# Kernel optimization log

Measured on AMD Instinct MI355X. Metric: run time of the kernel, lower is better.

Reference implementation:

```python
import jax, jax.numpy as jnp
import numpy as np

B, T, HE, L, HD = 512, 512, 512, 64, 512

def setup_inputs() -> dict:
    key = jax.random.key(0)
    ks = jax.random.split(key, 16)
    def w(k, shape):
        return jax.random.normal(k, shape, dtype=jnp.float32) * 0.05
    z32 = lambda n: jnp.zeros((n,), jnp.float32)
    return {
        "input_tensor": jax.random.normal(ks[0], (B, T, 1), dtype=jnp.float32),
        # encoder LSTMCell (keras gate order i, f, g, o)
        "enc_W": w(ks[1], (1, 4 * HE)),
        "enc_U": w(ks[2], (HE, 4 * HE)),
        "enc_b": z32(4 * HE),
        # encoder mu / std heads
        "emu_W": w(ks[3], (HE, L)), "emu_b": z32(L),
        "estd_W": w(ks[4], (HE, L)), "estd_b": z32(L),
        # decoder first-state dense (tanh)
        "dfs_W": w(ks[5], (L, HD)), "dfs_b": z32(HD),
        # decoder LSTMCell
        "dec_W": w(ks[6], (L, 4 * HD)),
        "dec_U": w(ks[7], (HD, 4 * HD)),
        "dec_b": z32(4 * HD),
        # decoder mu / std heads (Dense(1))
        "dmu_W": w(ks[8], (HD, 1)), "dmu_b": z32(1),
        "dstd_W": w(ks[9], (HD, 1)), "dstd_b": z32(1),
    }

def _lstm_update(gates, c):
    i, f, g, o = jnp.split(gates, 4, axis=-1)
    c_new = jax.nn.sigmoid(f) * c + jax.nn.sigmoid(i) * jnp.tanh(g)
    h_new = jax.nn.sigmoid(o) * jnp.tanh(c_new)
    return h_new, c_new

def reference(input_tensor, enc_W, enc_U, enc_b, emu_W, emu_b, estd_W, estd_b,
              dfs_W, dfs_b, dec_W, dec_U, dec_b, dmu_W, dmu_b, dstd_W, dstd_b):
    x = input_tensor
    Bn, Tn = x.shape[0], x.shape[1]
    He = enc_U.shape[0]

    # ---- encoder: LSTM over time, keep final h ----
    def enc_step(carry, xt):
        h, c = carry
        gates = xt @ enc_W + h @ enc_U + enc_b
        return _lstm_update(gates, c), None
    h0 = jnp.zeros((Bn, He), x.dtype)
    (hT, _), _ = jax.lax.scan(enc_step, (h0, h0), jnp.swapaxes(x, 0, 1))

    mu_enc = hT @ emu_W + emu_b                       # [B, L]
    sigma_enc = jax.nn.softplus(hT @ estd_W + estd_b)  # [B, L]
    z = mu_enc  # call() uses reparam=False -> latent returns mu

    # ---- decoder: LSTM fed constant z each step ----
    hd = jnp.tanh(z @ dfs_W + dfs_b)                  # [B, HD]
    cd = jnp.zeros_like(hd)
    zin = z @ dec_W + dec_b                           # input projection constant over t
    def dec_step(carry, _):
        h, c = carry
        h_new, c_new = _lstm_update(zin + h @ dec_U, c)
        mu = h_new @ dmu_W + dmu_b                    # [B, 1]
        sg = h_new @ dstd_W + dstd_b
        return (h_new, c_new), (mu, sg)
    _, (mus, sgs) = jax.lax.scan(dec_step, (hd, cd), None, length=Tn)

    mu_dec = jnp.swapaxes(mus, 0, 1)                  # [B, T, 1]
    sigma_dec = jax.nn.softplus(jnp.swapaxes(sgs, 0, 1))
    return (mu_dec, sigma_dec, mu_enc, sigma_enc)
```

## Files before the change

kernel.cpp:

```cpp
#include <hip/hip_runtime.h>


#define B_   512
#define T_   512
#define H_   512
#define NGR  32
#define WPG  8
#define RPG  16
#define UPW  64

typedef _Float16 f16;
typedef _Float16 f16x8 __attribute__((ext_vector_type(8)));
typedef _Float16 f16x4 __attribute__((ext_vector_type(4)));
typedef float f32x16 __attribute__((ext_vector_type(16)));
typedef unsigned long long u64;

#define OFF_SG_DEC 262144
#define OFF_MU_ENC 524288
#define OFF_SG_ENC 557056

__device__ __forceinline__ float sigm_(float x) { return 1.f / (1.f + __expf(-x)); }
__device__ __forceinline__ float tanh_(float x) {
  float t = fabsf(x);
  float e = __expf(2.f * t);
  float r = 1.f - 2.f / (e + 1.f);
  return x < 0.f ? -r : r;
}
__device__ __forceinline__ float softplus_(float x) {
  return fmaxf(x, 0.f) + log1pf(__expf(-fabsf(x)));
}

__global__ void pack_U(const float* __restrict__ U, f16* __restrict__ Upk) {
  const int e = blockIdx.x * 256 + threadIdx.x;
  const int j = e & 7, lane = (e >> 3) & 63, ks = (e >> 9) & 31;
  const int w = (e >> 14) & 7, wg = (e >> 17) & 7;
  const int ccol = lane & 31, khalf = lane >> 5;
  const int uu = ccol >> 2, gate = ccol & 3;
  const int k = ks * 16 + khalf * 8 + j;
  const int gcol = gate * 512 + wg * UPW + w * 8 + uu;
  Upk[e] = (f16)U[k * 2048 + gcol];
}

template <int IS_DEC>
__global__ void __launch_bounds__(512, 1)
lstm_rec(const f16* __restrict__ Upk,
         const float* __restrict__ xin,
         const float* __restrict__ wa,
         const float* __restrict__ wb,
         f16* __restrict__ hbuf,
         float* __restrict__ accmu,
         float* __restrict__ accsg,
         int* __restrict__ flags) {
  const int bid = blockIdx.x;
  const int wg = (bid >> 3) & 7;
  const int g = (bid & 7) * 4 + (bid >> 6);
  const int tid = threadIdx.x;
  const int wave = tid >> 6, lane = tid & 63;
  const int R0 = g * RPG;
  const int U0 = wg * UPW;

  const int ccol = lane & 31, khalf = lane >> 5;
  f16x8 Breg[32];
#pragma unroll
  for (int ks = 0; ks < 32; ++ks) {
    const f16* p = Upk + (((wg * 8 + wave) * 32 + ks) << 9) + lane * 8;
    asm volatile("global_load_dwordx4 %0, %1, off\n\ts_waitcnt vmcnt(0)"
                 : "=v"(Breg[ks]) : "v"(p));
  }

  const int row = tid >> 4;
  const int q = (tid & 15) * 4;
  float addv[16], xw[16], dmur[4], dstdr[4];
  if (tid < 256) {
#pragma unroll
    for (int m = 0; m < 4; ++m) {
#pragma unroll
      for (int gt = 0; gt < 4; ++gt) {
        const int col = gt * 512 + U0 + q + m;
        if (IS_DEC) {
          addv[m * 4 + gt] = xin[(R0 + row) * 2048 + col];
          xw[m * 4 + gt] = 0.f;
        } else {
          addv[m * 4 + gt] = wb[col];
          xw[m * 4 + gt] = wa[col];
        }
      }
      if (IS_DEC) {
        dmur[m] = wa[U0 + q + m];
        dstdr[m] = wb[U0 + q + m];
      } else {
        dmur[m] = 0.f;
        dstdr[m] = 0.f;
      }
    }
  }

  float cst[4] = {0.f, 0.f, 0.f, 0.f};

  __shared__ __align__(16) f16 hstage[RPG * 536];
  __shared__ float gatesLds[RPG * 260];
  __shared__ float xl[RPG * 516];

  if (!IS_DEC) {
#pragma unroll
    for (int i = 0; i < 16; ++i) {
      const int idx = tid + i * 512;
      const int r = idx >> 9, c2 = idx & 511;
      xl[r * 516 + c2] = xin[(R0 + r) * T_ + c2];
    }
    __syncthreads();
  }

  const int hrow = lane & 15;
  int* const myflag = &flags[(g * WPG + wg) * 32];
  int* const grpflags = &flags[(g * WPG) * 32];

  for (int t = 0; t < T_; ++t) {
    if (t) {
      for (;;) {
        int fv = t;
        if (lane < WPG)
          fv = __hip_atomic_load(&grpflags[lane * 32], __ATOMIC_RELAXED,
                                 __HIP_MEMORY_SCOPE_AGENT);
        if (__all(fv >= t)) break;
        asm volatile("s_sleep 1");
      }
    }

    const u64* hsrc64 = (const u64*)(hbuf + (t & 1) * (B_ * H_) + R0 * H_);
#pragma unroll
    for (int i = 0; i < 4; ++i) {
      const int w = tid + i * 512;
      const int r = w >> 7, c8 = w & 127;
      u64 v = __hip_atomic_load(hsrc64 + w, __ATOMIC_RELAXED,
                                __HIP_MEMORY_SCOPE_AGENT);
      *(u64*)&hstage[r * 536 + c8 * 4] = v;
    }
    __syncthreads();

    f32x16 acc;
#pragma unroll
    for (int j = 0; j < 16; ++j) acc[j] = 0.f;
#pragma unroll
    for (int ks = 0; ks < 32; ++ks) {
      f16x8 a = *(const f16x8*)&hstage[hrow * 536 + ks * 16 + khalf * 8];
      acc = __builtin_amdgcn_mfma_f32_32x32x16_f16(a, Breg[ks], acc, 0, 0, 0);
    }
#pragma unroll
    for (int r = 0; r < 8; ++r) {
      const int orow = (r & 3) + 8 * (r >> 2) + 4 * khalf;
      gatesLds[orow * 260 + wave * 32 + ccol] = acc[r];
    }
    __syncthreads();

    float hn[4];
    if (tid < 256) {
      float xv = 0.f;
      if (!IS_DEC) xv = xl[row * 516 + t];
#pragma unroll
      for (int m = 0; m < 4; ++m) {
        float ga[4];
#pragma unroll
        for (int gt = 0; gt < 4; ++gt) {
          float v = gatesLds[row * 260 + (q + m) * 4 + gt] + addv[m * 4 + gt];
          if (!IS_DEC) v += xv * xw[m * 4 + gt];
          ga[gt] = v;
        }
        const float iv = sigm_(ga[0]);
        const float fv = sigm_(ga[1]);
        const float gv = tanh_(ga[2]);
        const float ov = sigm_(ga[3]);
        const float cn = fv * cst[m] + iv * gv;
        cst[m] = cn;
        hn[m] = ov * tanh_(cn);
      }
      union { f16x4 h4; u64 u; } cv;
#pragma unroll
      for (int m = 0; m < 4; ++m) cv.h4[m] = (f16)hn[m];
      f16* hdst = hbuf + ((t + 1) & 1) * (B_ * H_) + (R0 + row) * H_ + U0 + q;
      __hip_atomic_store((u64*)hdst, cv.u, __ATOMIC_RELAXED,
                         __HIP_MEMORY_SCOPE_AGENT);
    }

    asm volatile("s_waitcnt vmcnt(0)" ::: "memory");
    __syncthreads();
    if (t + 1 < T_ && tid == 0)
      __hip_atomic_store(myflag, t + 1, __ATOMIC_RELAXED,
                         __HIP_MEMORY_SCOPE_AGENT);

    if (IS_DEC && tid < 256) {
      float pmu = 0.f, psg = 0.f;
#pragma unroll
      for (int m = 0; m < 4; ++m) {
        pmu += (float)((f16)hn[m]) * dmur[m];
        psg += (float)((f16)hn[m]) * dstdr[m];
      }
#pragma unroll
      for (int o = 1; o < 16; o <<= 1) {
        pmu += __shfl_xor(pmu, o);
        psg += __shfl_xor(psg, o);
      }
      if ((tid & 15) == 0) {
        unsafeAtomicAdd(&accmu[(R0 + row) * T_ + t], pmu);
        unsafeAtomicAdd(&accsg[(R0 + row) * T_ + t], psg);
      }
    }
  }
}

__global__ void enc_heads(const f16* __restrict__ h0, const float* __restrict__ emuW,
                          const float* __restrict__ emub, const float* __restrict__ estdW,
                          const float* __restrict__ estdb, float* __restrict__ out,
                          float* __restrict__ z) {
  const int b = blockIdx.x, tid = threadIdx.x;
  __shared__ float hrow[512];
  for (int k = tid; k < 512; k += 128)
    hrow[k] = (float)h0[b * H_ + k];
  __syncthreads();
  const int head = tid >> 6, l = tid & 63;
  const float* W = head ? estdW : emuW;
  float a = 0.f;
#pragma unroll 8
  for (int k = 0; k < 512; ++k) a += hrow[k] * W[k * 64 + l];
  if (head == 0) {
    const float v = a + emub[l];
    out[OFF_MU_ENC + b * 64 + l] = v;
    z[b * 64 + l] = v;
  } else {
    out[OFF_SG_ENC + b * 64 + l] = softplus_(a + estdb[l]);
  }
}

__global__ void dec_prep(const float* __restrict__ z, const float* __restrict__ dfsW,
                         const float* __restrict__ dfsb, const float* __restrict__ decW,
                         const float* __restrict__ decb, f16* __restrict__ hbuf,
                         float* __restrict__ zin) {
  const int b = blockIdx.x, tid = threadIdx.x;
  __shared__ float zl[64];
  if (tid < 64) zl[tid] = z[b * 64 + tid];
  __syncthreads();
  for (int c = tid; c < 512; c += 256) {
    float a = dfsb[c];
#pragma unroll
    for (int l = 0; l < 64; ++l) a += zl[l] * dfsW[l * 512 + c];
    hbuf[b * H_ + c] = (f16)tanh_(a);
  }
  for (int c = tid; c < 2048; c += 256) {
    float a = decb[c];
#pragma unroll
    for (int l = 0; l < 64; ++l) a += zl[l] * decW[l * 2048 + c];
    zin[b * 2048 + c] = a;
  }
}

__global__ void finalize_k(const float* __restrict__ accmu, const float* __restrict__ accsg,
                           const float* __restrict__ dmub, const float* __restrict__ dstdb,
                           float* __restrict__ out) {
  const int i = blockIdx.x * 256 + threadIdx.x;
  out[i] = accmu[i] + dmub[0];
  out[OFF_SG_DEC + i] = softplus_(accsg[i] + dstdb[0]);
}

extern "C" void kernel_launch(void* const* d_in, const int* in_sizes, int n_in,
                              void* d_out, int out_size, void* d_ws, size_t ws_size,
                              hipStream_t stream) {
  (void)in_sizes; (void)n_in; (void)out_size; (void)ws_size;
  const float* x     = (const float*)d_in[0];
  const float* encW  = (const float*)d_in[1];
  const float* encU  = (const float*)d_in[2];
  const float* encb  = (const float*)d_in[3];
  const float* emuW  = (const float*)d_in[4];
  const float* emub  = (const float*)d_in[5];
  const float* estdW = (const float*)d_in[6];
  const float* estdb = (const float*)d_in[7];
  const float* dfsW  = (const float*)d_in[8];
  const float* dfsb  = (const float*)d_in[9];
  const float* decW  = (const float*)d_in[10];
  const float* decU  = (const float*)d_in[11];
  const float* decb  = (const float*)d_in[12];
  const float* dmuW  = (const float*)d_in[13];
  const float* dmub  = (const float*)d_in[14];
  const float* dstdW = (const float*)d_in[15];
  const float* dstdb = (const float*)d_in[16];

  char* ws = (char*)d_ws;
  f16* hbuf    = (f16*)(ws + 0);
  float* accmu = (float*)(ws + (1u << 20));
  float* accsg = (float*)(ws + (2u << 20));
  int* flags   = (int*)(ws + (3u << 20));
  f16* UpkE    = (f16*)(ws + (3u << 20) + 65536);
  float* zin   = (float*)(ws + (3u << 20) + 65536);
  f16* UpkD    = (f16*)(ws + (7u << 20) + 65536);
  float* z     = (float*)(ws + (9u << 20) + 65536);
  float* out   = (float*)d_out;

  hipMemsetAsync(d_ws, 0, (3u << 20) + 65536, stream);

  hipLaunchKernelGGL(pack_U, dim3(4096), dim3(256), 0, stream, encU, UpkE);
  hipLaunchKernelGGL(pack_U, dim3(4096), dim3(256), 0, stream, decU, UpkD);

  hipLaunchKernelGGL((lstm_rec<0>), dim3(256), dim3(512), 0, stream,
                     UpkE, x, encW, encb, hbuf, (float*)nullptr, (float*)nullptr,
                     flags);
  hipLaunchKernelGGL(enc_heads, dim3(512), dim3(128), 0, stream,
                     hbuf, emuW, emub, estdW, estdb, out, z);
  hipLaunchKernelGGL(dec_prep, dim3(512), dim3(256), 0, stream,
                     z, dfsW, dfsb, decW, decb, hbuf, zin);
  hipLaunchKernelGGL((lstm_rec<1>), dim3(256), dim3(512), 0, stream,
                     UpkD, zin, dmuW, dstdW, hbuf, accmu, accsg, flags + 8192);
  hipLaunchKernelGGL(finalize_k, dim3(1024), dim3(256), 0, stream,
                     accmu, accsg, dmub, dstdb, out);
}
```

Before: 4.403 ms.

## Interleave two row groups per block to overlap flag waits with MFMA work

Each workgroup now handles two independent 16-row batch groups (A and B) and alternates between them. While one group's MFMA and gate math run, the block waits for and prefetches the other group's hidden state, which hides the cross-block flag spin and global h loads behind compute. The grid is halved from 256 to 128 blocks, so fewer CUs are used and each block does twice the serial work per timestep. Latency hiding could be outweighed by the longer per-step critical path.

```diff
diff --git a/kernel.cpp b/kernel.cpp
--- a/kernel.cpp
+++ b/kernel.cpp
@@ -4,7 +4,6 @@
 #define B_   512
 #define T_   512
 #define H_   512
-#define NGR  32
 #define WPG  8
 #define RPG  16
 #define UPW  64
@@ -53,24 +52,24 @@
          int* __restrict__ flags) {
   const int bid = blockIdx.x;
   const int wg = (bid >> 3) & 7;
-  const int g = (bid & 7) * 4 + (bid >> 6);
+  const int p = (bid & 7) * 2 + (bid >> 6);
+  const int RA = p * 16, RB = (p + 16) * 16;
   const int tid = threadIdx.x;
   const int wave = tid >> 6, lane = tid & 63;
-  const int R0 = g * RPG;
   const int U0 = wg * UPW;
 
   const int ccol = lane & 31, khalf = lane >> 5;
   f16x8 Breg[32];
 #pragma unroll
   for (int ks = 0; ks < 32; ++ks) {
-    const f16* p = Upk + (((wg * 8 + wave) * 32 + ks) << 9) + lane * 8;
+    const f16* ptr = Upk + (((wg * 8 + wave) * 32 + ks) << 9) + lane * 8;
     asm volatile("global_load_dwordx4 %0, %1, off\n\ts_waitcnt vmcnt(0)"
-                 : "=v"(Breg[ks]) : "v"(p));
+                 : "=v"(Breg[ks]) : "v"(ptr));
   }
 
   const int row = tid >> 4;
   const int q = (tid & 15) * 4;
-  float addv[16], xw[16], dmur[4], dstdr[4];
+  float addA[16], addB[16], xw[16], dmur[4], dstdr[4];
   if (tid < 256) {
 #pragma unroll
     for (int m = 0; m < 4; ++m) {
@@ -78,10 +77,12 @@
       for (int gt = 0; gt < 4; ++gt) {
         const int col = gt * 512 + U0 + q + m;
         if (IS_DEC) {
-          addv[m * 4 + gt] = xin[(R0 + row) * 2048 + col];
+          addA[m * 4 + gt] = xin[(RA + row) * 2048 + col];
+          addB[m * 4 + gt] = xin[(RB + row) * 2048 + col];
           xw[m * 4 + gt] = 0.f;
         } else {
-          addv[m * 4 + gt] = wb[col];
+          addA[m * 4 + gt] = wb[col];
+          addB[m * 4 + gt] = wb[col];
           xw[m * 4 + gt] = wa[col];
         }
       }
@@ -89,63 +90,81 @@
         dmur[m] = wa[U0 + q + m];
         dstdr[m] = wb[U0 + q + m];
       } else {
-        dmur[m] = 0.f;
-        dstdr[m] = 0.f;
-      }
-    }
-  }
-
-  float cst[4] = {0.f, 0.f, 0.f, 0.f};
-
-  __shared__ __align__(16) f16 hstage[RPG * 536];
+        dmur[m] = 0.f; dstdr[m] = 0.f;
+      }
+    }
+  }
+
+  float cstA[4] = {0.f, 0.f, 0.f, 0.f};
+  float cstB[4] = {0.f, 0.f, 0.f, 0.f};
+
+  __shared__ __align__(16) f16 bufA[RPG * 536];
+  __shared__ __align__(16) f16 bufB[RPG * 536];
   __shared__ float gatesLds[RPG * 260];
-  __shared__ float xl[RPG * 516];
+  __shared__ float xl[IS_DEC ? 4 : 32 * 516];
 
   if (!IS_DEC) {
 #pragma unroll
-    for (int i = 0; i < 16; ++i) {
+    for (int i = 0; i < 32; ++i) {
       const int idx = tid + i * 512;
       const int r = idx >> 9, c2 = idx & 511;
-      xl[r * 516 + c2] = xin[(R0 + r) * T_ + c2];
-    }
-    __syncthreads();
-  }
-
+      const int grow = (r < 16) ? (RA + r) : (RB + r - 16);
+      xl[r * 516 + c2] = xin[grow * T_ + c2];
+    }
+  }
+
+  int srow[4], scol[4], wof[4];
+#pragma unroll
+  for (int i = 0; i < 4; ++i) {
+    const int w = tid + i * 512;
+    srow[i] = w >> 7; scol[i] = w & 127;
+    wof[i] = w;
+  }
+  const u64* hb64 = (const u64*)hbuf;
+  const int baseA = RA * 128, baseB = RB * 128;
   const int hrow = lane & 15;
-  int* const myflag = &flags[(g * WPG + wg) * 32];
-  int* const grpflags = &flags[(g * WPG) * 32];
+
+  int* const flagA = &flags[(p * WPG + wg) * 32];
+  int* const flagB = &flags[((p + 16) * WPG + wg) * 32];
+  const int* const gfA = &flags[(p * WPG) * 32];
+  const int* const gfB = &flags[((p + 16) * WPG) * 32];
+
+#pragma unroll
+  for (int i = 0; i < 4; ++i) {
+    u64 v = __hip_atomic_load(hb64 + baseA + wof[i], __ATOMIC_RELAXED,
+                              __HIP_MEMORY_SCOPE_AGENT);
+    *(u64*)&bufA[srow[i] * 536 + scol[i] * 4] = v;
+  }
+  __syncthreads();
 
   for (int t = 0; t < T_; ++t) {
+    const int b0 = (t & 1) ? 65536 : 0;
+    const int b1 = (t & 1) ? 0 : 65536;
+    const int last = (t + 1 == T_);
+
+    f32x16 acc;
+#pragma unroll
+    for (int jj = 0; jj < 16; ++jj) acc[jj] = 0.f;
+#pragma unroll
+    for (int ks = 0; ks < 32; ++ks) {
+      f16x8 a = *(const f16x8*)&bufA[hrow * 536 + ks * 16 + khalf * 8];
+      acc = __builtin_amdgcn_mfma_f32_32x32x16_f16(a, Breg[ks], acc, 0, 0, 0);
+    }
     if (t) {
       for (;;) {
         int fv = t;
         if (lane < WPG)
-          fv = __hip_atomic_load(&grpflags[lane * 32], __ATOMIC_RELAXED,
+          fv = __hip_atomic_load(&gfB[lane * 32], __ATOMIC_RELAXED,
                                  __HIP_MEMORY_SCOPE_AGENT);
         if (__all(fv >= t)) break;
         asm volatile("s_sleep 1");
       }
     }
-
-    const u64* hsrc64 = (const u64*)(hbuf + (t & 1) * (B_ * H_) + R0 * H_);
-#pragma unroll
-    for (int i = 0; i < 4; ++i) {
-      const int w = tid + i * 512;
-      const int r = w >> 7, c8 = w & 127;
-      u64 v = __hip_atomic_load(hsrc64 + w, __ATOMIC_RELAXED,
+    u64 vB[4];
+#pragma unroll
+    for (int i = 0; i < 4; ++i)
+      vB[i] = __hip_atomic_load(hb64 + b0 + baseB + wof[i], __ATOMIC_RELAXED,
                                 __HIP_MEMORY_SCOPE_AGENT);
-      *(u64*)&hstage[r * 536 + c8 * 4] = v;
-    }
-    __syncthreads();
-
-    f32x16 acc;
-#pragma unroll
-    for (int j = 0; j < 16; ++j) acc[j] = 0.f;
-#pragma unroll
-    for (int ks = 0; ks < 32; ++ks) {
-      f16x8 a = *(const f16x8*)&hstage[hrow * 536 + ks * 16 + khalf * 8];
-      acc = __builtin_amdgcn_mfma_f32_32x32x16_f16(a, Breg[ks], acc, 0, 0, 0);
-    }
 #pragma unroll
     for (int r = 0; r < 8; ++r) {
       const int orow = (r & 3) + 8 * (r >> 2) + 4 * khalf;
@@ -153,7 +172,7 @@
     }
     __syncthreads();
 
-    float hn[4];
+    float hnA[4];
     if (tid < 256) {
       float xv = 0.f;
       if (!IS_DEC) xv = xl[row * 516 + t];
@@ -162,38 +181,35 @@
         float ga[4];
 #pragma unroll
         for (int gt = 0; gt < 4; ++gt) {
-          float v = gatesLds[row * 260 + (q + m) * 4 + gt] + addv[m * 4 + gt];
+          float v = gatesLds[row * 260 + (q + m) * 4 + gt] + addA[m * 4 + gt];
           if (!IS_DEC) v += xv * xw[m * 4 + gt];
           ga[gt] = v;
         }
-        const float iv = sigm_(ga[0]);
-        const float fv = sigm_(ga[1]);
-        const float gv = tanh_(ga[2]);
-        const float ov = sigm_(ga[3]);
-        const float cn = fv * cst[m] + iv * gv;
-        cst[m] = cn;
-        hn[m] = ov * tanh_(cn);
+        const float cn = sigm_(ga[1]) * cstA[m] + sigm_(ga[0]) * tanh_(ga[2]);
+        cstA[m] = cn;
+        hnA[m] = sigm_(ga[3]) * tanh_(cn);
       }
       union { f16x4 h4; u64 u; } cv;
 #pragma unroll
-      for (int m = 0; m < 4; ++m) cv.h4[m] = (f16)hn[m];
-      f16* hdst = hbuf + ((t + 1) & 1) * (B_ * H_) + (R0 + row) * H_ + U0 + q;
+      for (int m = 0; m < 4; ++m) cv.h4[m] = (f16)hnA[m];
+      f16* hdst = hbuf + ((t + 1) & 1) * (B_ * H_) + (RA + row) * H_ + U0 + q;
       __hip_atomic_store((u64*)hdst, cv.u, __ATOMIC_RELAXED,
                          __HIP_MEMORY_SCOPE_AGENT);
     }
-
+#pragma unroll
+    for (int i = 0; i < 4; ++i)
+      *(u64*)&bufB[srow[i] * 536 + scol[i] * 4] = vB[i];
     asm volatile("s_waitcnt vmcnt(0)" ::: "memory");
     __syncthreads();
-    if (t + 1 < T_ && tid == 0)
-      __hip_atomic_store(myflag, t + 1, __ATOMIC_RELAXED,
+    if (!last && tid == 0)
+      __hip_atomic_store(flagA, t + 1, __ATOMIC_RELAXED,
                          __HIP_MEMORY_SCOPE_AGENT);
-
     if (IS_DEC && tid < 256) {
       float pmu = 0.f, psg = 0.f;
 #pragma unroll
       for (int m = 0; m < 4; ++m) {
-        pmu += (float)((f16)hn[m]) * dmur[m];
-        psg += (float)((f16)hn[m]) * dstdr[m];
+        pmu += (float)((f16)hnA[m]) * dmur[m];
+        psg += (float)((f16)hnA[m]) * dstdr[m];
       }
 #pragma unroll
       for (int o = 1; o < 16; o <<= 1) {
@@ -201,8 +217,89 @@
         psg += __shfl_xor(psg, o);
       }
       if ((tid & 15) == 0) {
-        unsafeAtomicAdd(&accmu[(R0 + row) * T_ + t], pmu);
-        unsafeAtomicAdd(&accsg[(R0 + row) * T_ + t], psg);
+        unsafeAtomicAdd(&accmu[(RA + row) * T_ + t], pmu);
+        unsafeAtomicAdd(&accsg[(RA + row) * T_ + t], psg);
+      }
+    }
+
+#pragma unroll
+    for (int jj = 0; jj < 16; ++jj) acc[jj] = 0.f;
+#pragma unroll
+    for (int ks = 0; ks < 32; ++ks) {
+      f16x8 a = *(const f16x8*)&bufB[hrow * 536 + ks * 16 + khalf * 8];
+      acc = __builtin_amdgcn_mfma_f32_32x32x16_f16(a, Breg[ks], acc, 0, 0, 0);
+    }
+    u64 vA[4];
+    if (!last) {
+      for (;;) {
+        int fv = t + 1;
+        if (lane < WPG)
+          fv = __hip_atomic_load(&gfA[lane * 32], __ATOMIC_RELAXED,
+                                 __HIP_MEMORY_SCOPE_AGENT);
+        if (__all(fv >= t + 1)) break;
+        asm volatile("s_sleep 1");
+      }
+#pragma unroll
+      for (int i = 0; i < 4; ++i)
+        vA[i] = __hip_atomic_load(hb64 + b1 + baseA + wof[i], __ATOMIC_RELAXED,
+                                  __HIP_MEMORY_SCOPE_AGENT);
+    }
+#pragma unroll
+    for (int r = 0; r < 8; ++r) {
+      const int orow = (r & 3) + 8 * (r >> 2) + 4 * khalf;
+      gatesLds[orow * 260 + wave * 32 + ccol] = acc[r];
+    }
+    __syncthreads();
+
+    float hnB[4];
+    if (tid < 256) {
+      float xv = 0.f;
+      if (!IS_DEC) xv = xl[(16 + row) * 516 + t];
+#pragma unroll
+      for (int m = 0; m < 4; ++m) {
+        float ga[4];
+#pragma unroll
+        for (int gt = 0; gt < 4; ++gt) {
+          float v = gatesLds[row * 260 + (q + m) * 4 + gt] + addB[m * 4 + gt];
+          if (!IS_DEC) v += xv * xw[m * 4 + gt];
+          ga[gt] = v;
+        }
+        const float cn = sigm_(ga[1]) * cstB[m] + sigm_(ga[0]) * tanh_(ga[2]);
+        cstB[m] = cn;
+        hnB[m] = sigm_(ga[3]) * tanh_(cn);
+      }
+      union { f16x4 h4; u64 u; } cv;
+#pragma unroll
+      for (int m = 0; m < 4; ++m) cv.h4[m] = (f16)hnB[m];
+      f16* hdst = hbuf + ((t + 1) & 1) * (B_ * H_) + (RB + row) * H_ + U0 + q;
+      __hip_atomic_store((u64*)hdst, cv.u, __ATOMIC_RELAXED,
+                         __HIP_MEMORY_SCOPE_AGENT);
+    }
+    if (!last) {
+#pragma unroll
+      for (int i = 0; i < 4; ++i)
+        *(u64*)&bufA[srow[i] * 536 + scol[i] * 4] = vA[i];
+    }
+    asm volatile("s_waitcnt vmcnt(0)" ::: "memory");
+    __syncthreads();
+    if (!last && tid == 0)
+      __hip_atomic_store(flagB, t + 1, __ATOMIC_RELAXED,
+                         __HIP_MEMORY_SCOPE_AGENT);
+    if (IS_DEC && tid < 256) {
+      float pmu = 0.f, psg = 0.f;
+#pragma unroll
+      for (int m = 0; m < 4; ++m) {
+        pmu += (float)((f16)hnB[m]) * dmur[m];
+        psg += (float)((f16)hnB[m]) * dstdr[m];
+      }
+#pragma unroll
+      for (int o = 1; o < 16; o <<= 1) {
+        pmu += __shfl_xor(pmu, o);
+        psg += __shfl_xor(psg, o);
+      }
+      if ((tid & 15) == 0) {
+        unsafeAtomicAdd(&accmu[(RB + row) * T_ + t], pmu);
+        unsafeAtomicAdd(&accsg[(RB + row) * T_ + t], psg);
       }
     }
   }
@@ -299,14 +396,14 @@
   hipLaunchKernelGGL(pack_U, dim3(4096), dim3(256), 0, stream, encU, UpkE);
   hipLaunchKernelGGL(pack_U, dim3(4096), dim3(256), 0, stream, decU, UpkD);
 
-  hipLaunchKernelGGL((lstm_rec<0>), dim3(256), dim3(512), 0, stream,
+  hipLaunchKernelGGL((lstm_rec<0>), dim3(128), dim3(512), 0, stream,
                      UpkE, x, encW, encb, hbuf, (float*)nullptr, (float*)nullptr,
                      flags);
   hipLaunchKernelGGL(enc_heads, dim3(512), dim3(128), 0, stream,
                      hbuf, emuW, emub, estdW, estdb, out, z);
   hipLaunchKernelGGL(dec_prep, dim3(512), dim3(256), 0, stream,
                      z, dfsW, dfsb, decW, decb, hbuf, zin);
-  hipLaunchKernelGGL((lstm_rec<1>), dim3(256), dim3(512), 0, stream,
+  hipLaunchKernelGGL((lstm_rec<1>), dim3(128), dim3(512), 0, stream,
                      UpkD, zin, dmuW, dstdW, hbuf, accmu, accsg, flags + 8192);
   hipLaunchKernelGGL(finalize_k, dim3(1024), dim3(256), 0, stream,
                      accmu, accsg, dmub, dstdb, out);
```

New measurement: 5.408 ms. 1.23x slower.
